# Optimization experiments

Measured on AMD Instinct MI355X. Metric: run time of the kernel, lower is better.

The kernel has to match this reference:

```python
import jax, jax.numpy as jnp
import numpy as np

D_MODEL = 512
NUM_HEADS = 8
HEAD_DIM = D_MODEL // NUM_HEADS
LN_EPS = 1e-5


def setup_inputs() -> dict:
    key = jax.random.key(0)
    ks = jax.random.split(key, 12)
    B, S, D = 4, 8192, D_MODEL
    scale = 1.0 / np.sqrt(D)  # xavier-ish init
    inp = {
        "x": jax.random.normal(ks[0], (B, S, D), dtype=jnp.float32),
        "Wq": jax.random.normal(ks[1], (D, D), dtype=jnp.float32) * scale,
        "bq": jnp.zeros((D,), dtype=jnp.float32),
        "Wk": jax.random.normal(ks[2], (D, D), dtype=jnp.float32) * scale,
        "bk": jnp.zeros((D,), dtype=jnp.float32),
        "Wv": jax.random.normal(ks[3], (D, D), dtype=jnp.float32) * scale,
        "bv": jnp.zeros((D,), dtype=jnp.float32),
        "Wo": jax.random.normal(ks[4], (D, D), dtype=jnp.float32) * scale,
        "bo": jnp.zeros((D,), dtype=jnp.float32),
        "gamma": jnp.ones((D,), dtype=jnp.float32),
        "beta": jnp.zeros((D,), dtype=jnp.float32),
    }
    return inp


def _split_heads(t, B, S):
    # (B, S, D) -> (B, H, S, hd)
    return t.reshape(B, S, NUM_HEADS, HEAD_DIM).transpose(0, 2, 1, 3)


def _feature_map(t):
    return jax.nn.elu(t) + 1.0


def reference(x, Wq, bq, Wk, bk, Wv, bv, Wo, bo, gamma, beta):
    B, S, D = x.shape
    q = _split_heads(x @ Wq + bq, B, S)
    k = _split_heads(x @ Wk + bk, B, S)
    v = _split_heads(x @ Wv + bv, B, S)

    q = _feature_map(q)
    k = _feature_map(k)

    # kv summary: (B, H, hd, hd) -- O(n d^2) instead of O(n^2 d)
    kv = jnp.einsum('bhnd,bhnm->bhdm', k, v)
    out = jnp.einsum('bhnd,bhdm->bhnm', q, kv)

    k_sum = k.sum(axis=2)  # (B, H, hd)
    normalizer = jnp.clip(jnp.einsum('bhnd,bhd->bhn', q, k_sum), 1e-6, None)
    out = out / normalizer[..., None]

    # merge heads: (B, H, S, hd) -> (B, S, D)
    out = out.transpose(0, 2, 1, 3).reshape(B, S, D)
    out = out @ Wo + bo

    # residual + layer norm (dropout is identity in eval / p=0)
    y = x + out
    mean = y.mean(axis=-1, keepdims=True)
    var = y.var(axis=-1, keepdims=True)
    y = (y - mean) * jax.lax.rsqrt(var + LN_EPS)
    return y * gamma + beta
```

## Files before the change

### kernel.cpp

```cpp
#include <hip/hip_runtime.h>
#include <cstdint>

#define SEQ     8192
#define BATCH   4
#define NHEAD   8
#define NTOK    (BATCH*SEQ)

typedef __bf16 bf16x8 __attribute__((ext_vector_type(8)));
typedef float  floatx4 __attribute__((ext_vector_type(4)));

static __device__ __forceinline__ float b2f(uint16_t h) {
    return __uint_as_float(((uint32_t)h) << 16);
}
static __device__ __forceinline__ uint16_t f2b(float f) {
    uint32_t u = __float_as_uint(f);
    u += 0x7fffu + ((u >> 16) & 1u);
    return (uint16_t)(u >> 16);
}

static __device__ __forceinline__ void async_copy16(const uint16_t* g, uint16_t* l) {
#if __has_builtin(__builtin_amdgcn_global_load_lds)
    __builtin_amdgcn_global_load_lds(
        (const __attribute__((address_space(1))) void*)g,
        (__attribute__((address_space(3))) void*)l, 16, 0, 0);
#else
    *(uint4*)l = *(const uint4*)g;
#endif
}

__global__ __launch_bounds__(256) void convert_x(
    const float* __restrict__ X, uint16_t* __restrict__ Xb)
{
    const size_t i = ((size_t)blockIdx.x * 256 + threadIdx.x) * 8;
    float4 f0 = *(const float4*)(X + i);
    float4 f1 = *(const float4*)(X + i + 4);
    uint4 o;
    uint16_t* p = (uint16_t*)&o;
    p[0]=f2b(f0.x); p[1]=f2b(f0.y); p[2]=f2b(f0.z); p[3]=f2b(f0.w);
    p[4]=f2b(f1.x); p[5]=f2b(f1.y); p[6]=f2b(f1.z); p[7]=f2b(f1.w);
    *(uint4*)(Xb + i) = o;
}

__global__ __launch_bounds__(256) void convert_w(
    const float* __restrict__ Wq, const float* __restrict__ Wk,
    const float* __restrict__ Wv, const float* __restrict__ Wo,
    uint16_t* __restrict__ out)
{
    const int z = blockIdx.z;
    const float* W = (z == 0) ? Wq : (z == 1) ? Wk : (z == 2) ? Wv : Wo;
    uint16_t* o = out + (size_t)z * 262144;
    const int n0 = blockIdx.x * 64, k0 = blockIdx.y * 64;
    __shared__ uint16_t tl[64][64];
    const int t = threadIdx.x;
    const int r  = t >> 4;
    const int c4 = (t & 15) * 4;
    #pragma unroll
    for (int s = 0; s < 4; ++s) {
        const int k = r + s * 16;
        float4 f = *(const float4*)(W + (size_t)(k0 + k) * 512 + n0 + c4);
        tl[c4 + 0][k] = f2b(f.x); tl[c4 + 1][k] = f2b(f.y);
        tl[c4 + 2][k] = f2b(f.z); tl[c4 + 3][k] = f2b(f.w);
    }
    __syncthreads();
    const int n  = t >> 2;
    const int kk = (t & 3) * 16;
    uint4* dst = (uint4*)(o + (size_t)(n0 + n) * 512 + k0 + kk);
    dst[0] = *(const uint4*)&tl[n][kk];
    dst[1] = *(const uint4*)&tl[n][kk + 8];
}

__global__ __launch_bounds__(256) void qkv128(
    const uint16_t* __restrict__ Xb,
    const uint16_t* __restrict__ Wt,
    const float* __restrict__ bq_, const float* __restrict__ bk_,
    const float* __restrict__ bv_,
    uint16_t* __restrict__ outQ, uint16_t* __restrict__ outK,
    uint16_t* __restrict__ outV)
{
    const int id = blockIdx.x;
    const int c  = id & 7;
    const int r_ = id >> 3;
    const int j_ = r_ % 12;
    const int s  = (r_ / 12) * 8 + c;
    const int proj = j_ >> 2;
    const int n0   = (j_ & 3) * 128;
    const int m0   = s * 128;

    const uint16_t* W = Wt + (size_t)proj * 262144;
    const float* bias = (proj == 0) ? bq_ : (proj == 1) ? bk_ : bv_;
    uint16_t* out     = (proj == 0) ? outQ : (proj == 1) ? outK : outV;
    const int act = (proj < 2);

    __shared__ uint16_t smem[24576];
    const int t = threadIdx.x;
    const int wave = t >> 6, lane = t & 63, quad = lane >> 4, lrow = lane & 15;
    const int wm = (wave & 1) * 64, wn = (wave >> 1) * 64;
    const int sr = t >> 2;
    const int scz = ((t & 3) ^ ((t >> 3) & 3)) * 8;

    const uint16_t* gA = Xb + (size_t)(m0 + sr) * 512 + scz;
    const uint16_t* gB = W  + (size_t)(n0 + sr) * 512 + scz;

    floatx4 acc[4][4] = {};

    auto STAGE = [&](int st, int bi) {
        const uint16_t* pA = gA + st * 32;
        uint16_t* d = smem + bi * 8192;
        async_copy16(pA,            d + t * 8);
        async_copy16(pA + 64 * 512, d + (t + 256) * 8);
        const uint16_t* pB = gB + st * 32;
        async_copy16(pB,            d + 4096 + t * 8);
        async_copy16(pB + 64 * 512, d + 4096 + (t + 256) * 8);
    };
    const int gsl = (quad ^ ((lrow >> 1) & 3)) * 8;
    auto COMPUTE = [&](int bi) {
        const uint16_t* base = smem + bi * 8192;
        bf16x8 af[4], bfr[4];
        #pragma unroll
        for (int i = 0; i < 4; ++i)
            af[i] = *(const bf16x8*)(base + (wm + i * 16 + lrow) * 32 + gsl);
        #pragma unroll
        for (int j = 0; j < 4; ++j)
            bfr[j] = *(const bf16x8*)(base + 4096 + (wn + j * 16 + lrow) * 32 + gsl);
        #pragma unroll
        for (int i = 0; i < 4; ++i)
            #pragma unroll
            for (int j = 0; j < 4; ++j)
                acc[i][j] = __builtin_amdgcn_mfma_f32_16x16x32_bf16(af[i], bfr[j], acc[i][j], 0, 0, 0);
    };

    STAGE(0, 0);
    STAGE(1, 1);

    int cb = 0, sb = 2;
    for (int i = 0; i < 14; ++i) {
        STAGE(i + 2, sb);
        asm volatile("s_waitcnt vmcnt(8)" ::: "memory");
        __builtin_amdgcn_s_barrier();
        __builtin_amdgcn_sched_barrier(0);
        COMPUTE(cb);
        __builtin_amdgcn_s_barrier();
        cb = (cb == 2) ? 0 : cb + 1;
        sb = (sb == 2) ? 0 : sb + 1;
    }
    asm volatile("s_waitcnt vmcnt(4)" ::: "memory");
    __builtin_amdgcn_s_barrier();
    __builtin_amdgcn_sched_barrier(0);
    COMPUTE(cb);
    __builtin_amdgcn_s_barrier();
    asm volatile("s_waitcnt vmcnt(0)" ::: "memory");
    __builtin_amdgcn_s_barrier();
    __builtin_amdgcn_sched_barrier(0);
    COMPUTE(0);
    __syncthreads();

    #pragma unroll
    for (int j = 0; j < 4; ++j) {
        const int col = wn + j * 16 + lrow;
        const float bb = bias[n0 + col];
        #pragma unroll
        for (int i = 0; i < 4; ++i) {
            #pragma unroll
            for (int r = 0; r < 4; ++r) {
                const int row = wm + i * 16 + quad * 4 + r;
                float v = acc[i][j][r] + bb;
                if (act) v = (v > 0.0f) ? (v + 1.0f) : __expf(v);
                smem[row * 128 + (col ^ (((row >> 2) & 3) << 4))] = f2b(v);
            }
        }
    }
    __syncthreads();
    #pragma unroll
    for (int p = 0; p < 8; ++p) {
        const int idx = p * 256 + t;
        const int row = idx >> 4;
        const int cc  = (idx & 15) * 8;
        uint4 v = *(const uint4*)(smem + row * 128 + (cc ^ (((row >> 2) & 3) << 4)));
        *(uint4*)(out + (size_t)(m0 + row) * 512 + n0 + cc) = v;
    }
}

__global__ __launch_bounds__(256) void gemm_out128(
    const uint16_t* __restrict__ A,
    const uint16_t* __restrict__ Wt,
    const float* __restrict__ bias,
    const float* __restrict__ resid,
    uint16_t* __restrict__ out)
{
    const int id = blockIdx.x;
    const int c  = id & 7;
    const int r_ = id >> 3;
    const int j_ = r_ & 3;
    const int s  = (r_ >> 2) * 8 + c;
    const int n0 = j_ * 128;
    const int m0 = s * 128;

    __shared__ uint16_t smem[16384];
    const int t = threadIdx.x;
    const int wave = t >> 6, lane = t & 63, quad = lane >> 4, lrow = lane & 15;
    const int wm = (wave & 1) * 64, wn = (wave >> 1) * 64;
    const int sr = t >> 2;
    const int scz = ((t & 3) ^ ((t >> 3) & 3)) * 8;

    const uint16_t* gA = A  + (size_t)(m0 + sr) * 512 + scz;
    const uint16_t* gB = Wt + (size_t)(n0 + sr) * 512 + scz;

    floatx4 acc[4][4] = {};

    async_copy16(gA,            smem + t * 8);
    async_copy16(gA + 64 * 512, smem + (t + 256) * 8);
    async_copy16(gB,            smem + 4096 + t * 8);
    async_copy16(gB + 64 * 512, smem + 4096 + (t + 256) * 8);
    __syncthreads();

    const int gsl = (quad ^ ((lrow >> 1) & 3)) * 8;
    int cur = 0;
    for (int k0 = 0; k0 < 512; k0 += 32) {
        const int nxt = cur ^ 1;
        if (k0 + 32 < 512) {
            const uint16_t* pA = gA + k0 + 32;
            async_copy16(pA,            smem + nxt * 8192 + t * 8);
            async_copy16(pA + 64 * 512, smem + nxt * 8192 + (t + 256) * 8);
            const uint16_t* pB = gB + k0 + 32;
            async_copy16(pB,            smem + nxt * 8192 + 4096 + t * 8);
            async_copy16(pB + 64 * 512, smem + nxt * 8192 + 4096 + (t + 256) * 8);
        }
        const uint16_t* base = smem + cur * 8192;
        bf16x8 af[4], bfr[4];
        #pragma unroll
        for (int i = 0; i < 4; ++i)
            af[i] = *(const bf16x8*)(base + (wm + i * 16 + lrow) * 32 + gsl);
        #pragma unroll
        for (int j = 0; j < 4; ++j)
            bfr[j] = *(const bf16x8*)(base + 4096 + (wn + j * 16 + lrow) * 32 + gsl);
        #pragma unroll
        for (int i = 0; i < 4; ++i)
            #pragma unroll
            for (int j = 0; j < 4; ++j)
                acc[i][j] = __builtin_amdgcn_mfma_f32_16x16x32_bf16(af[i], bfr[j], acc[i][j], 0, 0, 0);
        __syncthreads();
        cur = nxt;
    }

    #pragma unroll
    for (int j = 0; j < 4; ++j) {
        const int col = wn + j * 16 + lrow;
        const float bb = bias[n0 + col];
        #pragma unroll
        for (int i = 0; i < 4; ++i) {
            #pragma unroll
            for (int r = 0; r < 4; ++r) {
                const int row = wm + i * 16 + quad * 4 + r;
                float v = acc[i][j][r] + bb
                        + resid[(size_t)(m0 + row) * 512 + n0 + col];
                smem[row * 128 + (col ^ (((row >> 2) & 3) << 4))] = f2b(v);
            }
        }
    }
    __syncthreads();
    #pragma unroll
    for (int p = 0; p < 8; ++p) {
        const int idx = p * 256 + t;
        const int row = idx >> 4;
        const int cc  = (idx & 15) * 8;
        uint4 v = *(const uint4*)(smem + row * 128 + (cc ^ (((row >> 2) & 3) << 4)));
        *(uint4*)(out + (size_t)(m0 + row) * 512 + n0 + cc) = v;
    }
}

__global__ __launch_bounds__(256) void kv_accum(
    const uint16_t* __restrict__ K,
    const uint16_t* __restrict__ V,
    float* __restrict__ KV,
    float* __restrict__ KSUM)
{
    const int chunk = blockIdx.x;
    const int h     = blockIdx.y;
    const int b     = blockIdx.z;
    const int t    = threadIdx.x;
    const int wv   = t >> 6;
    const int lane = t & 63;
    const int quad = lane >> 4;
    const int lrow = lane & 15;

    __shared__ uint16_t kt[64 * 66];
    __shared__ uint16_t vt[64 * 66];

    floatx4 acc[4] = {};
    floatx4 accS = {};
    union { uint16_t u[8]; bf16x8 v; } one_u;
    #pragma unroll
    for (int j = 0; j < 8; ++j) one_u.u[j] = 0x3F80;
    const bf16x8 ones = one_u.v;

    const size_t base = ((size_t)(b * SEQ + chunk * 512)) * 512 + h * 64;

    for (int n0 = 0; n0 < 512; n0 += 64) {
        #pragma unroll
        for (int s = 0; s < 2; ++s) {
            const int i   = t + 256 * s;
            const int tok = i >> 3;
            const int d0  = (i & 7) * 8;
            uint4 kq = *(const uint4*)(K + base + (size_t)(n0 + tok) * 512 + d0);
            const uint16_t* kp = (const uint16_t*)&kq;
            #pragma unroll
            for (int j = 0; j < 8; ++j) kt[(d0 + j) * 66 + tok] = kp[j];
            uint4 vq = *(const uint4*)(V + base + (size_t)(n0 + tok) * 512 + d0);
            const uint16_t* vp = (const uint16_t*)&vq;
            #pragma unroll
            for (int j = 0; j < 8; ++j) vt[(d0 + j) * 66 + tok] = vp[j];
        }
        __syncthreads();
        #pragma unroll
        for (int ks = 0; ks < 2; ++ks) {
            bf16x8 af = *(const bf16x8*)(kt + (wv * 16 + lrow) * 66 + ks * 32 + quad * 8);
            accS = __builtin_amdgcn_mfma_f32_16x16x32_bf16(af, ones, accS, 0, 0, 0);
            #pragma unroll
            for (int nt = 0; nt < 4; ++nt) {
                bf16x8 bf = *(const bf16x8*)(vt + (nt * 16 + lrow) * 66 + ks * 32 + quad * 8);
                acc[nt] = __builtin_amdgcn_mfma_f32_16x16x32_bf16(af, bf, acc[nt], 0, 0, 0);
            }
        }
        __syncthreads();
    }

    float* kvp = KV + (size_t)(b * NHEAD + h) * 4096;
    #pragma unroll
    for (int nt = 0; nt < 4; ++nt) {
        const int m = nt * 16 + lrow;
        #pragma unroll
        for (int r = 0; r < 4; ++r) {
            const int d = wv * 16 + quad * 4 + r;
            atomicAdd(kvp + d * 64 + m, acc[nt][r]);
        }
    }
    if (lrow == 0) {
        float* kp = KSUM + (size_t)(b * NHEAD + h) * 64;
        #pragma unroll
        for (int r = 0; r < 4; ++r)
            atomicAdd(kp + wv * 16 + quad * 4 + r, accS[r]);
    }
}

__global__ __launch_bounds__(256) void attn_apply(
    const uint16_t* __restrict__ Q,
    const float* __restrict__ KVg,
    const float* __restrict__ KSg,
    uint16_t* __restrict__ OUT)
{
    const int h    = blockIdx.y;
    const int tok0 = blockIdx.x * 64;
    const int b    = tok0 >> 13;
    const int t    = threadIdx.x;
    const int wv   = t >> 6;
    const int lane = t & 63;
    const int quad = lane >> 4;
    const int lrow = lane & 15;

    __shared__ uint16_t bt[64 * 66];
    __shared__ uint16_t ksb[64];

    const float* kvp = KVg + (size_t)(b * NHEAD + h) * 4096;
    #pragma unroll
    for (int s = 0; s < 16; ++s) {
        const int e = t + 256 * s;
        const int d = e >> 6, m = e & 63;
        bt[m * 66 + d] = f2b(kvp[e]);
    }
    if (t < 64) ksb[t] = f2b(KSg[(size_t)(b * NHEAD + h) * 64 + t]);
    __syncthreads();

    floatx4 acc[4] = {};
    floatx4 accN = {};
    const uint16_t* qrow = Q + (size_t)(tok0 + wv * 16 + lrow) * 512 + h * 64 + quad * 8;
    #pragma unroll
    for (int ks = 0; ks < 2; ++ks) {
        bf16x8 af = *(const bf16x8*)(qrow + ks * 32);
        bf16x8 bks = *(const bf16x8*)(ksb + ks * 32 + quad * 8);
        accN = __builtin_amdgcn_mfma_f32_16x16x32_bf16(af, bks, accN, 0, 0, 0);
        #pragma unroll
        for (int nt = 0; nt < 4; ++nt) {
            bf16x8 bf = *(const bf16x8*)(bt + (nt * 16 + lrow) * 66 + ks * 32 + quad * 8);
            acc[nt] = __builtin_amdgcn_mfma_f32_16x16x32_bf16(af, bf, acc[nt], 0, 0, 0);
        }
    }

    __syncthreads();
    #pragma unroll
    for (int r = 0; r < 4; ++r) {
        const float inv = 1.0f / fmaxf(accN[r], 1e-6f);
        const int row = wv * 16 + quad * 4 + r;
        #pragma unroll
        for (int nt = 0; nt < 4; ++nt) {
            const int col = nt * 16 + lrow;
            bt[row * 64 + (col ^ (((row >> 2) & 3) << 4))] = f2b(acc[nt][r] * inv);
        }
    }
    __syncthreads();
    #pragma unroll
    for (int p = 0; p < 2; ++p) {
        const int idx = p * 256 + t;
        const int row = idx >> 3;
        const int cc  = (idx & 7) * 8;
        uint4 v = *(const uint4*)(bt + row * 64 + (cc ^ (((row >> 2) & 3) << 4)));
        *(uint4*)(OUT + (size_t)(tok0 + row) * 512 + h * 64 + cc) = v;
    }
}

__global__ __launch_bounds__(256) void ln_rows(
    const uint16_t* __restrict__ Z,
    const float* __restrict__ gamma,
    const float* __restrict__ beta,
    float* __restrict__ OUT)
{
    const int t = threadIdx.x;
    const int wv = t >> 6, lane = t & 63;
    const size_t row = (size_t)blockIdx.x * 4 + wv;
    union { uint4 q; uint16_t u[8]; } zz;
    zz.q = *(const uint4*)(Z + row * 512 + lane * 8);
    float v[8], s = 0.f, s2 = 0.f;
    #pragma unroll
    for (int j = 0; j < 8; ++j) {
        v[j] = b2f(zz.u[j]);
        s += v[j]; s2 += v[j] * v[j];
    }
    #pragma unroll
    for (int off = 32; off > 0; off >>= 1) {
        s  += __shfl_xor(s, off, 64);
        s2 += __shfl_xor(s2, off, 64);
    }
    const float mean = s * (1.0f / 512.0f);
    const float var  = s2 * (1.0f / 512.0f) - mean * mean;
    const float inv  = rsqrtf(var + 1e-5f);
    float4 g0 = *(const float4*)(gamma + lane * 8);
    float4 g1 = *(const float4*)(gamma + lane * 8 + 4);
    float4 b0 = *(const float4*)(beta + lane * 8);
    float4 b1 = *(const float4*)(beta + lane * 8 + 4);
    float4 o0, o1;
    o0.x = (v[0]-mean)*inv*g0.x + b0.x;  o0.y = (v[1]-mean)*inv*g0.y + b0.y;
    o0.z = (v[2]-mean)*inv*g0.z + b0.z;  o0.w = (v[3]-mean)*inv*g0.w + b0.w;
    o1.x = (v[4]-mean)*inv*g1.x + b1.x;  o1.y = (v[5]-mean)*inv*g1.y + b1.y;
    o1.z = (v[6]-mean)*inv*g1.z + b1.z;  o1.w = (v[7]-mean)*inv*g1.w + b1.w;
    *(float4*)(OUT + row * 512 + lane * 8)     = o0;
    *(float4*)(OUT + row * 512 + lane * 8 + 4) = o1;
}

extern "C" void kernel_launch(void* const* d_in, const int* in_sizes, int n_in,
                              void* d_out, int out_size, void* d_ws, size_t ws_size,
                              hipStream_t stream)
{
    (void)in_sizes; (void)n_in; (void)out_size; (void)ws_size;
    const float* x     = (const float*)d_in[0];
    const float* Wq    = (const float*)d_in[1];
    const float* bq    = (const float*)d_in[2];
    const float* Wk    = (const float*)d_in[3];
    const float* bk    = (const float*)d_in[4];
    const float* Wv    = (const float*)d_in[5];
    const float* bv    = (const float*)d_in[6];
    const float* Wo    = (const float*)d_in[7];
    const float* bo    = (const float*)d_in[8];
    const float* gamma = (const float*)d_in[9];
    const float* beta  = (const float*)d_in[10];

    uint8_t* ws = (uint8_t*)d_ws;
    float*    KV   = (float*)ws;
    float*    KSUM = (float*)(ws + (size_t)32 * 4096 * 4);
    uint16_t* Wt   = (uint16_t*)(ws + (size_t)32 * 4096 * 4 + 32 * 64 * 4);
    uint16_t* phiQ = (uint16_t*)(ws + (size_t)32 * 4096 * 4 + 32 * 64 * 4
                                    + (size_t)4 * 262144 * 2);
    uint16_t* Xb   = phiQ + (size_t)NTOK * 512;
    uint16_t* phiK = (uint16_t*)d_out;
    uint16_t* vbuf = (uint16_t*)d_out + (size_t)NTOK * 512;
    uint16_t* attn = Xb;
    uint16_t* zbuf = phiQ;

    hipMemsetAsync(ws, 0, (size_t)32 * 4096 * 4 + 32 * 64 * 4, stream);

    dim3 blk(256);
    convert_x<<<dim3(NTOK * 512 / (256 * 8)), blk, 0, stream>>>(x, Xb);
    convert_w<<<dim3(8, 8, 4), blk, 0, stream>>>(Wq, Wk, Wv, Wo, Wt);
    qkv128<<<dim3(3072), blk, 0, stream>>>(
        Xb, Wt, bq, bk, bv, phiQ, phiK, vbuf);
    kv_accum<<<dim3(16, NHEAD, BATCH), blk, 0, stream>>>(phiK, vbuf, KV, KSUM);
    attn_apply<<<dim3(NTOK / 64, NHEAD), blk, 0, stream>>>(phiQ, KV, KSUM, attn);
    gemm_out128<<<dim3(1024), blk, 0, stream>>>(
        attn, Wt + (size_t)3 * 262144, bo, x, zbuf);
    ln_rows<<<dim3(NTOK / 4), blk, 0, stream>>>(zbuf, gamma, beta, (float*)d_out);
}
```

Before: 279.5 us.

## Store K/V transposed per head, async double-buffer kv_accum, prep bf16 KV once

The QKV projection epilogue now writes phi(K) and V transposed into a per-(batch,head) [d][token] layout, so kv_accum can stream tiles with 16-byte async global-to-LDS copies into double-buffered, XOR-swizzled shared memory. This replaces the scalar transposing LDS stores. The KV accumulation is stored transposed, and a new small kernel converts KV and KSUM to bf16 in swizzled order once. attn_apply then just async-copies that tile instead of every block converting fp32 itself. This adds a kernel launch, and the K/V epilogue stores become strided across rows of length SEQ.

```diff
diff --git a/kernel.cpp b/kernel.cpp
--- a/kernel.cpp
+++ b/kernel.cpp
@@ -74,8 +74,9 @@
     const uint16_t* __restrict__ Wt,
     const float* __restrict__ bq_, const float* __restrict__ bk_,
     const float* __restrict__ bv_,
-    uint16_t* __restrict__ outQ, uint16_t* __restrict__ outK,
-    uint16_t* __restrict__ outV)
+    uint16_t* __restrict__ outQ,
+    uint16_t* __restrict__ outKt,
+    uint16_t* __restrict__ outVt)
 {
     const int id = blockIdx.x;
     const int c  = id & 7;
@@ -88,7 +89,6 @@
 
     const uint16_t* W = Wt + (size_t)proj * 262144;
     const float* bias = (proj == 0) ? bq_ : (proj == 1) ? bk_ : bv_;
-    uint16_t* out     = (proj == 0) ? outQ : (proj == 1) ? outK : outV;
     const int act = (proj < 2);
 
     __shared__ uint16_t smem[24576];
@@ -154,29 +154,61 @@
     COMPUTE(0);
     __syncthreads();
 
-    #pragma unroll
-    for (int j = 0; j < 4; ++j) {
-        const int col = wn + j * 16 + lrow;
-        const float bb = bias[n0 + col];
-        #pragma unroll
-        for (int i = 0; i < 4; ++i) {
+    if (proj == 0) {
+        #pragma unroll
+        for (int j = 0; j < 4; ++j) {
+            const int col = wn + j * 16 + lrow;
+            const float bb = bias[n0 + col];
             #pragma unroll
-            for (int r = 0; r < 4; ++r) {
-                const int row = wm + i * 16 + quad * 4 + r;
-                float v = acc[i][j][r] + bb;
-                if (act) v = (v > 0.0f) ? (v + 1.0f) : __expf(v);
-                smem[row * 128 + (col ^ (((row >> 2) & 3) << 4))] = f2b(v);
+            for (int i = 0; i < 4; ++i) {
+                #pragma unroll
+                for (int r = 0; r < 4; ++r) {
+                    const int row = wm + i * 16 + quad * 4 + r;
+                    float v = acc[i][j][r] + bb;
+                    v = (v > 0.0f) ? (v + 1.0f) : __expf(v);
+                    smem[row * 128 + (col ^ (((row >> 2) & 3) << 4))] = f2b(v);
+                }
             }
         }
-    }
-    __syncthreads();
-    #pragma unroll
-    for (int p = 0; p < 8; ++p) {
-        const int idx = p * 256 + t;
-        const int row = idx >> 4;
-        const int cc  = (idx & 15) * 8;
-        uint4 v = *(const uint4*)(smem + row * 128 + (cc ^ (((row >> 2) & 3) << 4)));
-        *(uint4*)(out + (size_t)(m0 + row) * 512 + n0 + cc) = v;
+        __syncthreads();
+        #pragma unroll
+        for (int p = 0; p < 8; ++p) {
+            const int idx = p * 256 + t;
+            const int row = idx >> 4;
+            const int cc  = (idx & 15) * 8;
+            uint4 v = *(const uint4*)(smem + row * 128 + (cc ^ (((row >> 2) & 3) << 4)));
+            *(uint4*)(outQ + (size_t)(m0 + row) * 512 + n0 + cc) = v;
+        }
+    } else {
+        uint16_t* out = (proj == 1) ? outKt : outVt;
+        #pragma unroll
+        for (int j = 0; j < 4; ++j) {
+            const int col = wn + j * 16 + lrow;
+            const float bb = bias[n0 + col];
+            #pragma unroll
+            for (int i = 0; i < 4; ++i) {
+                #pragma unroll
+                for (int r = 0; r < 4; ++r) {
+                    const int tok = wm + i * 16 + quad * 4 + r;
+                    float v = acc[i][j][r] + bb;
+                    if (act) v = (v > 0.0f) ? (v + 1.0f) : __expf(v);
+                    smem[col * 128 + (tok ^ ((col & 7) << 3))] = f2b(v);
+                }
+            }
+        }
+        __syncthreads();
+        const int b_  = m0 >> 13;
+        const int ti0 = m0 & 8191;
+        #pragma unroll
+        for (int p = 0; p < 8; ++p) {
+            const int idx = p * 256 + t;
+            const int col = idx >> 4;
+            const int tg  = (idx & 15) * 8;
+            uint4 v = *(const uint4*)(smem + col * 128 + (tg ^ ((col & 7) << 3)));
+            const int nc = n0 + col;
+            const int h_ = nc >> 6, d_ = nc & 63;
+            *(uint4*)(out + (((size_t)b_ * NHEAD + h_) * 64 + d_) * SEQ + ti0 + tg) = v;
+        }
     }
 }
 
@@ -269,22 +301,22 @@
 }
 
 __global__ __launch_bounds__(256) void kv_accum(
-    const uint16_t* __restrict__ K,
-    const uint16_t* __restrict__ V,
+    const uint16_t* __restrict__ Kt,
+    const uint16_t* __restrict__ Vt,
     float* __restrict__ KV,
     float* __restrict__ KSUM)
 {
     const int chunk = blockIdx.x;
     const int h     = blockIdx.y;
     const int b     = blockIdx.z;
+    const int bh    = b * NHEAD + h;
     const int t    = threadIdx.x;
     const int wv   = t >> 6;
     const int lane = t & 63;
     const int quad = lane >> 4;
     const int lrow = lane & 15;
 
-    __shared__ uint16_t kt[64 * 66];
-    __shared__ uint16_t vt[64 * 66];
+    __shared__ uint16_t smem[32768];
 
     floatx4 acc[4] = {};
     floatx4 accS = {};
@@ -293,81 +325,104 @@
     for (int j = 0; j < 8; ++j) one_u.u[j] = 0x3F80;
     const bf16x8 ones = one_u.v;
 
-    const size_t base = ((size_t)(b * SEQ + chunk * 512)) * 512 + h * 64;
-
-    for (int n0 = 0; n0 < 512; n0 += 64) {
-        #pragma unroll
-        for (int s = 0; s < 2; ++s) {
-            const int i   = t + 256 * s;
-            const int tok = i >> 3;
-            const int d0  = (i & 7) * 8;
-            uint4 kq = *(const uint4*)(K + base + (size_t)(n0 + tok) * 512 + d0);
-            const uint16_t* kp = (const uint16_t*)&kq;
-            #pragma unroll
-            for (int j = 0; j < 8; ++j) kt[(d0 + j) * 66 + tok] = kp[j];
-            uint4 vq = *(const uint4*)(V + base + (size_t)(n0 + tok) * 512 + d0);
-            const uint16_t* vp = (const uint16_t*)&vq;
-            #pragma unroll
-            for (int j = 0; j < 8; ++j) vt[(d0 + j) * 66 + tok] = vp[j];
-        }
-        __syncthreads();
-        #pragma unroll
-        for (int ks = 0; ks < 2; ++ks) {
-            bf16x8 af = *(const bf16x8*)(kt + (wv * 16 + lrow) * 66 + ks * 32 + quad * 8);
+    const size_t rowbase = (size_t)bh * 64;
+    const int tok0 = chunk * 512;
+    const int r_st = t >> 4;
+    const int g_st = t & 15;
+
+    auto STAGE = [&](int tt, int bi) {
+        uint16_t* dK = smem + bi * 16384;
+        const int tb = tok0 + tt * 128;
+        #pragma unroll
+        for (int m = 0; m < 4; ++m) {
+            const int r  = r_st + m * 16;
+            const int gs = g_st ^ (r & 7);
+            async_copy16(Kt + (rowbase + r) * SEQ + tb + gs * 8, dK + m * 2048 + t * 8);
+            async_copy16(Vt + (rowbase + r) * SEQ + tb + gs * 8, dK + 8192 + m * 2048 + t * 8);
+        }
+    };
+
+    STAGE(0, 0);
+    __syncthreads();
+
+    int cur = 0;
+    for (int tt = 0; tt < 4; ++tt) {
+        if (tt < 3) STAGE(tt + 1, cur ^ 1);
+        const uint16_t* kb = smem + cur * 16384;
+        const uint16_t* vb = kb + 8192;
+        #pragma unroll
+        for (int ks = 0; ks < 4; ++ks) {
+            const int gp = ((ks * 4 + quad) ^ (lrow & 7)) * 8;
+            bf16x8 af = *(const bf16x8*)(kb + (wv * 16 + lrow) * 128 + gp);
             accS = __builtin_amdgcn_mfma_f32_16x16x32_bf16(af, ones, accS, 0, 0, 0);
             #pragma unroll
             for (int nt = 0; nt < 4; ++nt) {
-                bf16x8 bf = *(const bf16x8*)(vt + (nt * 16 + lrow) * 66 + ks * 32 + quad * 8);
+                bf16x8 bf = *(const bf16x8*)(vb + (nt * 16 + lrow) * 128 + gp);
                 acc[nt] = __builtin_amdgcn_mfma_f32_16x16x32_bf16(af, bf, acc[nt], 0, 0, 0);
             }
         }
         __syncthreads();
-    }
-
-    float* kvp = KV + (size_t)(b * NHEAD + h) * 4096;
+        cur ^= 1;
+    }
+
+    float* kvp = KV + (size_t)bh * 4096;
     #pragma unroll
     for (int nt = 0; nt < 4; ++nt) {
         const int m = nt * 16 + lrow;
         #pragma unroll
         for (int r = 0; r < 4; ++r) {
             const int d = wv * 16 + quad * 4 + r;
-            atomicAdd(kvp + d * 64 + m, acc[nt][r]);
+            atomicAdd(kvp + m * 64 + d, acc[nt][r]);
         }
     }
     if (lrow == 0) {
-        float* kp = KSUM + (size_t)(b * NHEAD + h) * 64;
+        float* kp = KSUM + (size_t)bh * 64;
         #pragma unroll
         for (int r = 0; r < 4; ++r)
             atomicAdd(kp + wv * 16 + quad * 4 + r, accS[r]);
     }
 }
 
+__global__ __launch_bounds__(256) void kvb_prep(
+    const float* __restrict__ KV, const float* __restrict__ KSUM,
+    uint16_t* __restrict__ KVb, uint16_t* __restrict__ KSb)
+{
+    const int bh = blockIdx.x;
+    const int t = threadIdx.x;
+    const float* src = KV + (size_t)bh * 4096;
+    uint16_t* dst = KVb + (size_t)bh * 4096;
+    #pragma unroll
+    for (int j = 0; j < 16; ++j) {
+        const int idx = t + 256 * j;
+        const int m = idx >> 6, d = idx & 63;
+        dst[m * 64 + (((d >> 3) ^ (m & 7)) * 8) + (d & 7)] = f2b(src[idx]);
+    }
+    if (t < 64) KSb[bh * 64 + t] = f2b(KSUM[(size_t)bh * 64 + t]);
+}
+
 __global__ __launch_bounds__(256) void attn_apply(
     const uint16_t* __restrict__ Q,
-    const float* __restrict__ KVg,
-    const float* __restrict__ KSg,
+    const uint16_t* __restrict__ KVb,
+    const uint16_t* __restrict__ KSb,
     uint16_t* __restrict__ OUT)
 {
     const int h    = blockIdx.y;
     const int tok0 = blockIdx.x * 64;
     const int b    = tok0 >> 13;
+    const int bh   = b * NHEAD + h;
     const int t    = threadIdx.x;
     const int wv   = t >> 6;
     const int lane = t & 63;
     const int quad = lane >> 4;
     const int lrow = lane & 15;
 
-    __shared__ uint16_t bt[64 * 66];
+    __shared__ uint16_t bt[4096];
     __shared__ uint16_t ksb[64];
 
-    const float* kvp = KVg + (size_t)(b * NHEAD + h) * 4096;
-    #pragma unroll
-    for (int s = 0; s < 16; ++s) {
-        const int e = t + 256 * s;
-        const int d = e >> 6, m = e & 63;
-        bt[m * 66 + d] = f2b(kvp[e]);
-    }
-    if (t < 64) ksb[t] = f2b(KSg[(size_t)(b * NHEAD + h) * 64 + t]);
+    const uint16_t* src = KVb + (size_t)bh * 4096;
+    async_copy16(src + t * 8,        bt + t * 8);
+    async_copy16(src + 2048 + t * 8, bt + 2048 + t * 8);
+    if (t < 64) ksb[t] = KSb[(size_t)bh * 64 + t];
     __syncthreads();
 
     floatx4 acc[4] = {};
@@ -380,7 +435,8 @@
         accN = __builtin_amdgcn_mfma_f32_16x16x32_bf16(af, bks, accN, 0, 0, 0);
         #pragma unroll
         for (int nt = 0; nt < 4; ++nt) {
-            bf16x8 bf = *(const bf16x8*)(bt + (nt * 16 + lrow) * 66 + ks * 32 + quad * 8);
+            const int gp = ((ks * 4 + quad) ^ (lrow & 7)) * 8;
+            bf16x8 bf = *(const bf16x8*)(bt + (nt * 16 + lrow) * 64 + gp);
             acc[nt] = __builtin_amdgcn_mfma_f32_16x16x32_bf16(af, bf, acc[nt], 0, 0, 0);
         }
     }
@@ -469,8 +525,10 @@
     uint16_t* phiQ = (uint16_t*)(ws + (size_t)32 * 4096 * 4 + 32 * 64 * 4
                                     + (size_t)4 * 262144 * 2);
     uint16_t* Xb   = phiQ + (size_t)NTOK * 512;
-    uint16_t* phiK = (uint16_t*)d_out;
-    uint16_t* vbuf = (uint16_t*)d_out + (size_t)NTOK * 512;
+    uint16_t* Kt   = (uint16_t*)d_out;
+    uint16_t* Vt   = Kt + (size_t)NTOK * 512;
+    uint16_t* KVb  = (uint16_t*)d_out;
+    uint16_t* KSb  = KVb + (size_t)32 * 4096;
     uint16_t* attn = Xb;
     uint16_t* zbuf = phiQ;
 
@@ -480,9 +538,10 @@
     convert_x<<<dim3(NTOK * 512 / (256 * 8)), blk, 0, stream>>>(x, Xb);
     convert_w<<<dim3(8, 8, 4), blk, 0, stream>>>(Wq, Wk, Wv, Wo, Wt);
     qkv128<<<dim3(3072), blk, 0, stream>>>(
-        Xb, Wt, bq, bk, bv, phiQ, phiK, vbuf);
-    kv_accum<<<dim3(16, NHEAD, BATCH), blk, 0, stream>>>(phiK, vbuf, KV, KSUM);
-    attn_apply<<<dim3(NTOK / 64, NHEAD), blk, 0, stream>>>(phiQ, KV, KSUM, attn);
+        Xb, Wt, bq, bk, bv, phiQ, Kt, Vt);
+    kv_accum<<<dim3(16, NHEAD, BATCH), blk, 0, stream>>>(Kt, Vt, KV, KSUM);
+    kvb_prep<<<dim3(32), blk, 0, stream>>>(KV, KSUM, KVb, KSb);
+    attn_apply<<<dim3(NTOK / 64, NHEAD), blk, 0, stream>>>(phiQ, KVb, KSb, attn);
     gemm_out128<<<dim3(1024), blk, 0, stream>>>(
         attn, Wt + (size_t)3 * 262144, bo, x, zbuf);
     ln_rows<<<dim3(NTOK / 4), blk, 0, stream>>>(zbuf, gamma, beta, (float*)d_out);
```

Result: slower. 300.6 us (+7.6%).
